# Performance work log

Hardware: AMD Instinct MI355X
Metric: run time of the kernel (lower is better)

Reference implementation:

```python
import jax, jax.numpy as jnp
import numpy as np

N = 100000   # nodes
B = 64       # graphs in batch
E = 1600000  # edges
D_IN = 2
W1D = W2D = W3D = 128
N_CLASSES = 3
MIN_SCORE = 0.1
TOL = 1e-7
BN_EPS = 1e-5


def setup_inputs() -> dict:
    key = jax.random.key(0)
    ks = jax.random.split(key, 32)
    inp = {}
    inp['x'] = jax.random.normal(ks[0], (N, D_IN), jnp.float32)
    inp['edge_index'] = jax.random.randint(ks[1], (2, E), 0, N, dtype=jnp.int32)
    inp['batch_index'] = jnp.sort(jax.random.randint(ks[2], (N,), 0, B, dtype=jnp.int32))
    inp['topk_w'] = jax.random.normal(ks[3], (D_IN,), jnp.float32)
    dims = [(D_IN, W1D), (W1D, W2D), (W2D, W3D)]
    k = 4
    for i, (din, dout) in enumerate(dims, start=1):
        inp[f'W{i}'] = jax.random.normal(ks[k], (din, dout), jnp.float32) * (1.0 / np.sqrt(din)); k += 1
        inp[f'b{i}'] = jax.random.normal(ks[k], (dout,), jnp.float32) * 0.05; k += 1
        inp[f'g{i}'] = 1.0 + 0.1 * jax.random.normal(ks[k], (dout,), jnp.float32); k += 1
        inp[f'be{i}'] = 0.1 * jax.random.normal(ks[k], (dout,), jnp.float32); k += 1
        inp[f'rm{i}'] = 0.1 * jax.random.normal(ks[k], (dout,), jnp.float32); k += 1
        inp[f'rv{i}'] = 1.0 + 0.1 * jax.random.uniform(ks[k], (dout,), jnp.float32); k += 1
    inp['linW'] = jax.random.normal(ks[k], (W3D, N_CLASSES), jnp.float32) * (1.0 / np.sqrt(W3D)); k += 1
    inp['linb'] = jax.random.normal(ks[k], (N_CLASSES,), jnp.float32) * 0.05
    return inp


def _bn_eval(x, g, be, rm, rv):
    # BatchNorm1d in eval mode (running stats)
    return (x - rm) * jax.lax.rsqrt(rv + BN_EPS) * g + be


def _gcn(x, src, dst, ew, W, b):
    # GCNConv: lin -> symmetric-normalized scatter-add (self-loops already in src/dst/ew)
    xw = x @ W                                   # [N, dout]
    deg = jax.ops.segment_sum(ew, dst, num_segments=N)
    dinv = jnp.where(deg > 0, jax.lax.rsqrt(deg), 0.0)
    norm = dinv[src] * ew * dinv[dst]            # [E+N]
    out = jax.ops.segment_sum(norm[:, None] * xw[src], dst, num_segments=N)
    return out + b


def reference(x, edge_index, batch_index, topk_w,
              W1, b1, g1, be1, rm1, rv1,
              W2, b2, g2, be2, rm2, rv2,
              W3, b3, g3, be3, rm3, rv3,
              linW, linb):
    # ---- TopKPooling (min_score mode): per-graph softmax score, threshold keep,
    # x scaled by score. Implemented via masking (fixed shapes): dropped nodes get
    # zero features, zero edge weights, and -inf at the max pool -> math identical
    # to PyG's node filtering (BN is eval-mode, i.e. per-node).
    logits = x @ topk_w                                                    # [N]
    m = jax.ops.segment_max(logits, batch_index, num_segments=B)
    e = jnp.exp(logits - m[batch_index])
    score = e / jax.ops.segment_sum(e, batch_index, num_segments=B)[batch_index]
    smax = jax.ops.segment_max(score, batch_index, num_segments=B)[batch_index] - TOL
    keep = score > jnp.minimum(smax, MIN_SCORE)                            # [N] bool
    keep_f = keep.astype(x.dtype)
    h = x * (score * keep_f)[:, None]

    src0, dst0 = edge_index[0], edge_index[1]
    loop = jnp.arange(N, dtype=src0.dtype)
    src = jnp.concatenate([src0, loop])
    dst = jnp.concatenate([dst0, loop])
    ew = jnp.concatenate([keep_f[src0] * keep_f[dst0], keep_f])            # mask + self-loops

    h = _bn_eval(jax.nn.relu(_gcn(h, src, dst, ew, W1, b1)), g1, be1, rm1, rv1)
    h = _bn_eval(jax.nn.relu(_gcn(h, src, dst, ew, W2, b2)), g2, be2, rm2, rv2)
    h = _bn_eval(jax.nn.relu(_gcn(h, src, dst, ew, W3, b3)), g3, be3, rm3, rv3)

    neg = jnp.finfo(h.dtype).min
    h = jnp.where(keep[:, None], h, neg)
    pooled = jax.ops.segment_max(h, batch_index, num_segments=B)           # [B, w3]
    out = pooled @ linW + linb
    return jax.nn.log_softmax(out, axis=1)
```

## Files before the change

### kernel.cpp

```cpp
#include <hip/hip_runtime.h>
#include <hip/hip_bf16.h>

#define NN 100000
#define BB 64
#define EE 1600000
#define FD 128
#define KMAX 8192
#define EMAX (1 << 18)

__device__ __forceinline__ unsigned encf(float f) {
    unsigned u = __float_as_uint(f);
    return (u & 0x80000000u) ? ~u : (u | 0x80000000u);
}
__device__ __forceinline__ float decf(unsigned u) {
    return __uint_as_float((u & 0x80000000u) ? (u & 0x7FFFFFFFu) : ~u);
}

struct InitBlk {
    unsigned menc[BB];
    float    ssum[BB];
    unsigned smenc[BB];
    int      kcnt;
    int      kecnt;
    int      pad[2];
    unsigned pooled[BB * FD];
};

__global__ void k_score1(const float* __restrict__ x, const float* __restrict__ tw,
                         const int* __restrict__ bidx, float* __restrict__ sc, InitBlk* ib) {
    __shared__ unsigned lm[BB];
    if (threadIdx.x < BB) lm[threadIdx.x] = 0u;
    __syncthreads();
    int i = blockIdx.x * 256 + threadIdx.x;
    if (i < NN) {
        float l = x[2 * i] * tw[0] + x[2 * i + 1] * tw[1];
        sc[i] = l;
        atomicMax(&lm[bidx[i]], encf(l));
    }
    __syncthreads();
    if (threadIdx.x < BB && lm[threadIdx.x] != 0u)
        atomicMax(&ib->menc[threadIdx.x], lm[threadIdx.x]);
}

__global__ void k_score2(const int* __restrict__ bidx, float* __restrict__ sc, InitBlk* ib) {
    __shared__ float ls[BB];
    if (threadIdx.x < BB) ls[threadIdx.x] = 0.f;
    __syncthreads();
    int i = blockIdx.x * 256 + threadIdx.x;
    if (i < NN) {
        int b = bidx[i];
        float e = expf(sc[i] - decf(ib->menc[b]));
        sc[i] = e;
        atomicAdd(&ls[b], e);
    }
    __syncthreads();
    if (threadIdx.x < BB && ls[threadIdx.x] != 0.f)
        atomicAdd(&ib->ssum[threadIdx.x], ls[threadIdx.x]);
}

__global__ void k_score3(const int* __restrict__ bidx, float* __restrict__ sc, InitBlk* ib) {
    __shared__ unsigned lm[BB];
    if (threadIdx.x < BB) lm[threadIdx.x] = 0u;
    __syncthreads();
    int i = blockIdx.x * 256 + threadIdx.x;
    if (i < NN) {
        int b = bidx[i];
        float s = sc[i] / ib->ssum[b];
        sc[i] = s;
        atomicMax(&lm[b], encf(s));
    }
    __syncthreads();
    if (threadIdx.x < BB && lm[threadIdx.x] != 0u)
        atomicMax(&ib->smenc[threadIdx.x], lm[threadIdx.x]);
}

__global__ void k_keep(const float* __restrict__ x, const int* __restrict__ bidx,
                       const float* __restrict__ sc, unsigned char* __restrict__ kf,
                       int* __restrict__ nslot, int* __restrict__ bslot,
                       float* __restrict__ degs, float* __restrict__ h0s,
                       float* __restrict__ ps, InitBlk* ib) {
    int i = blockIdx.x * 256 + threadIdx.x;
    if (i >= NN) return;
    int b = bidx[i];
    float thr = fminf(decf(ib->smenc[b]) - 1e-7f, 0.1f);
    float s = sc[i];
    bool kp = s > thr;
    int idx = -1;
    if (kp) {
        idx = atomicAdd(&ib->kcnt, 1);
        if (idx >= KMAX) kp = false;
    }
    kf[i] = kp ? 1 : 0;
    if (kp) {
        nslot[i] = idx;
        bslot[idx] = b;
        degs[idx] = 1.0f;
        h0s[2 * idx]     = x[2 * i] * s;
        h0s[2 * idx + 1] = x[2 * i + 1] * s;
        ps[2 * idx] = 0.f; ps[2 * idx + 1] = 0.f;
    }
}

__global__ void k_edges(const int* __restrict__ ei, const unsigned char* __restrict__ kf,
                        const int* __restrict__ nslot, float* __restrict__ degs,
                        int* __restrict__ kedge, InitBlk* ib) {
    int e = blockIdx.x * 256 + threadIdx.x;
    if (e >= EE) return;
    int s = ei[e], d = ei[EE + e];
    if ((kf[s] & kf[d]) != 0) {
        int ds = nslot[d];
        atomicAdd(&degs[ds], 1.0f);
        int idx = atomicAdd(&ib->kecnt, 1);
        if (idx < EMAX) { kedge[2 * idx] = nslot[s]; kedge[2 * idx + 1] = ds; }
    }
}

__global__ void k_dinv(float* __restrict__ degs, const InitBlk* ib) {
    int n = ib->kcnt; if (n > KMAX) n = KMAX;
    for (int t = blockIdx.x * blockDim.x + threadIdx.x; t < n; t += gridDim.x * blockDim.x)
        degs[t] = rsqrtf(degs[t]);
}

__global__ void k_l1edge(const float* __restrict__ dinv, const float* __restrict__ h0s,
                         float* __restrict__ ps, const int* __restrict__ kedge, const InitBlk* ib) {
    int n = ib->kecnt; if (n > EMAX) n = EMAX;
    for (int t = blockIdx.x * blockDim.x + threadIdx.x; t < n; t += gridDim.x * blockDim.x) {
        int s = kedge[2 * t], d = kedge[2 * t + 1];
        float nm = dinv[s] * dinv[d];
        atomicAdd(&ps[2 * d],     nm * h0s[2 * s]);
        atomicAdd(&ps[2 * d + 1], nm * h0s[2 * s + 1]);
    }
}

__global__ void k_l1node(const float* __restrict__ ps, const float* __restrict__ h0s,
                         const float* __restrict__ dinv,
                         const float* __restrict__ W1, const float* __restrict__ b1,
                         const float* __restrict__ g1, const float* __restrict__ be1,
                         const float* __restrict__ rm1, const float* __restrict__ rv1,
                         const InitBlk* ib, float* __restrict__ hout) {
    int kc = ib->kcnt; if (kc > KMAX) kc = KMAX;
    int n = kc * FD;
    for (int t = blockIdx.x * blockDim.x + threadIdx.x; t < n; t += gridDim.x * blockDim.x) {
        int slot = t >> 7, f = t & 127;
        float di = dinv[slot], d2 = di * di;
        float a0 = ps[2 * slot]     + d2 * h0s[2 * slot];
        float a1 = ps[2 * slot + 1] + d2 * h0s[2 * slot + 1];
        float v = a0 * W1[f] + a1 * W1[FD + f] + b1[f];
        v = fmaxf(v, 0.f);
        v = (v - rm1[f]) * rsqrtf(rv1[f] + 1e-5f) * g1[f] + be1[f];
        hout[t] = v;
    }
}

__global__ void k_mm(float* __restrict__ X, float* __restrict__ Y, const float* __restrict__ W,
                     const InitBlk* ib) {
    __shared__ float row[FD];
    int n = ib->kcnt; if (n > KMAX) n = KMAX;
    for (int slot = blockIdx.x; slot < n; slot += gridDim.x) {
        size_t base = (size_t)slot * FD;
        row[threadIdx.x] = X[base + threadIdx.x];
        X[base + threadIdx.x] = 0.f;
        __syncthreads();
        float acc = 0.f;
        #pragma unroll 16
        for (int k = 0; k < FD; k++) acc += row[k] * W[k * FD + threadIdx.x];
        Y[base + threadIdx.x] = acc;
        __syncthreads();
    }
}

__global__ void k_scatter(const float* __restrict__ Y, float* __restrict__ X,
                          const float* __restrict__ dinv, const int* __restrict__ kedge,
                          const InitBlk* ib) {
    int n = ib->kecnt; if (n > EMAX) n = EMAX;
    for (int t = blockIdx.x * blockDim.x + threadIdx.x; t < n; t += gridDim.x * blockDim.x) {
        int s = kedge[2 * t], d = kedge[2 * t + 1];
        float nm = dinv[s] * dinv[d];
        const float* ys = Y + (size_t)s * FD;
        float* xd = X + (size_t)d * FD;
        for (int f = 0; f < FD; f += 4) {
            float4 v = *(const float4*)(ys + f);
            atomicAdd(xd + f,     nm * v.x);
            atomicAdd(xd + f + 1, nm * v.y);
            atomicAdd(xd + f + 2, nm * v.z);
            atomicAdd(xd + f + 3, nm * v.w);
        }
    }
}

__global__ void k_bn(const float* __restrict__ X, float* __restrict__ Y,
                     const float* __restrict__ dinv,
                     const float* __restrict__ bb, const float* __restrict__ g,
                     const float* __restrict__ be, const float* __restrict__ rm,
                     const float* __restrict__ rv, const InitBlk* ib) {
    int kc = ib->kcnt; if (kc > KMAX) kc = KMAX;
    int n = kc * FD;
    for (int t = blockIdx.x * blockDim.x + threadIdx.x; t < n; t += gridDim.x * blockDim.x) {
        int slot = t >> 7, f = t & 127;
        float di = dinv[slot];
        float v = X[t] + di * di * Y[t] + bb[f];
        v = fmaxf(v, 0.f);
        v = (v - rm[f]) * rsqrtf(rv[f] + 1e-5f) * g[f] + be[f];
        Y[t] = v;
    }
}

__global__ void k_pool(const float* __restrict__ H, const int* __restrict__ bslot, InitBlk* ib) {
    int kc = ib->kcnt; if (kc > KMAX) kc = KMAX;
    int n = kc * FD;
    for (int t = blockIdx.x * blockDim.x + threadIdx.x; t < n; t += gridDim.x * blockDim.x) {
        int slot = t >> 7, f = t & 127;
        atomicMax(&ib->pooled[bslot[slot] * FD + f], encf(H[t]));
    }
}

__global__ void k_final(const InitBlk* __restrict__ ib, const float* __restrict__ linW,
                        const float* __restrict__ linb, float* __restrict__ out) {
    int b = threadIdx.x;
    if (b >= BB) return;
    float z0 = linb[0], z1 = linb[1], z2 = linb[2];
    for (int f = 0; f < FD; f++) {
        unsigned u = ib->pooled[b * FD + f];
        float pv = (u == 0u) ? -3.4028235e38f : decf(u);
        z0 += pv * linW[f * 3 + 0];
        z1 += pv * linW[f * 3 + 1];
        z2 += pv * linW[f * 3 + 2];
    }
    float m = fmaxf(z0, fmaxf(z1, z2));
    float l = m + logf(expf(z0 - m) + expf(z1 - m) + expf(z2 - m));
    out[b * 3 + 0] = z0 - l;
    out[b * 3 + 1] = z1 - l;
    out[b * 3 + 2] = z2 - l;
}

extern "C" void kernel_launch(void* const* d_in, const int* in_sizes, int n_in,
                              void* d_out, int out_size, void* d_ws, size_t ws_size,
                              hipStream_t stream) {
    (void)in_sizes; (void)n_in; (void)out_size; (void)ws_size;
    const float* x    = (const float*)d_in[0];
    const int*   ei   = (const int*)d_in[1];
    const int*   bidx = (const int*)d_in[2];
    const float* tw   = (const float*)d_in[3];
    const float* W1 = (const float*)d_in[4],  *b1 = (const float*)d_in[5],  *g1 = (const float*)d_in[6];
    const float* be1= (const float*)d_in[7],  *rm1= (const float*)d_in[8],  *rv1= (const float*)d_in[9];
    const float* W2 = (const float*)d_in[10], *b2 = (const float*)d_in[11], *g2 = (const float*)d_in[12];
    const float* be2= (const float*)d_in[13], *rm2= (const float*)d_in[14], *rv2= (const float*)d_in[15];
    const float* W3 = (const float*)d_in[16], *b3 = (const float*)d_in[17], *g3 = (const float*)d_in[18];
    const float* be3= (const float*)d_in[19], *rm3= (const float*)d_in[20], *rv3= (const float*)d_in[21];
    const float* linW = (const float*)d_in[22], *linb = (const float*)d_in[23];
    float* out = (float*)d_out;

    char* w = (char*)d_ws;
    auto take = [&](size_t bytes) { char* r = w; w += (bytes + 255) & ~(size_t)255; return r; };
    InitBlk* ib = (InitBlk*)take(sizeof(InitBlk));
    float* sc    = (float*)take((size_t)NN * 4);
    unsigned char* kf = (unsigned char*)take(NN);
    int*   nslot = (int*)take((size_t)NN * 4);
    int*   bslot = (int*)take((size_t)KMAX * 4);
    float* degs  = (float*)take((size_t)KMAX * 4);
    float* h0s   = (float*)take((size_t)KMAX * 8);
    float* ps    = (float*)take((size_t)KMAX * 8);
    int*   kedge = (int*)take((size_t)EMAX * 8);
    float* hA    = (float*)take((size_t)KMAX * FD * 4);
    float* hB    = (float*)take((size_t)KMAX * FD * 4);

    hipMemsetAsync(ib, 0, sizeof(InitBlk), stream);

    int nb = (NN + 255) / 256;
    int eb = (EE + 255) / 256;
    k_score1<<<nb, 256, 0, stream>>>(x, tw, bidx, sc, ib);
    k_score2<<<nb, 256, 0, stream>>>(bidx, sc, ib);
    k_score3<<<nb, 256, 0, stream>>>(bidx, sc, ib);
    k_keep  <<<nb, 256, 0, stream>>>(x, bidx, sc, kf, nslot, bslot, degs, h0s, ps, ib);
    k_edges <<<eb, 256, 0, stream>>>(ei, kf, nslot, degs, kedge, ib);
    k_dinv  <<<32, 256, 0, stream>>>(degs, ib);
    k_l1edge<<<32, 256, 0, stream>>>(degs, h0s, ps, kedge, ib);
    k_l1node<<<64, 256, 0, stream>>>(ps, h0s, degs, W1, b1, g1, be1, rm1, rv1, ib, hA);
    k_mm     <<<128, 128, 0, stream>>>(hA, hB, W2, ib);
    k_scatter<<<64, 256, 0, stream>>>(hB, hA, degs, kedge, ib);
    k_bn     <<<64, 256, 0, stream>>>(hA, hB, degs, b2, g2, be2, rm2, rv2, ib);
    k_mm     <<<128, 128, 0, stream>>>(hB, hA, W3, ib);
    k_scatter<<<64, 256, 0, stream>>>(hA, hB, degs, kedge, ib);
    k_bn     <<<64, 256, 0, stream>>>(hB, hA, degs, b3, g3, be3, rm3, rv3, ib);
    k_pool   <<<64, 256, 0, stream>>>(hA, bslot, ib);
    k_final  <<<1, 64, 0, stream>>>(ib, linW, linb, out);
}
```

Measured before the change: 176.4 us.

## Collapse pipeline into three kernels: per-graph score/keep block and single-block tail

Replaces the sixteen-launch pipeline with three kernels. One block per graph computes the softmax scores, threshold and kept-node list using binary search over the sorted batch index and a shared-memory cache. A single 1024-thread block then runs all three GCN layers, pooling and the final linear layer with block-level syncs. Kept nodes get fixed per-graph slots (capped at 64 per graph), which removes the global counters, the memset and most launch overhead. In exchange the tail runs on one CU, so it is fast only while few nodes and edges are kept, and any graph keeping more than 64 nodes would give a wrong result.

```diff
diff --git a/kernel.cpp b/kernel.cpp
--- a/kernel.cpp
+++ b/kernel.cpp
@@ -5,8 +5,10 @@
 #define BB 64
 #define EE 1600000
 #define FD 128
-#define KMAX 8192
+#define SLOTC 64
+#define KSLOTS (BB * SLOTC)
 #define EMAX (1 << 18)
+#define LCAP 12288
 
 __device__ __forceinline__ unsigned encf(float f) {
     unsigned u = __float_as_uint(f);
@@ -16,221 +18,218 @@
     return __uint_as_float((u & 0x80000000u) ? (u & 0x7FFFFFFFu) : ~u);
 }
 
-struct InitBlk {
-    unsigned menc[BB];
-    float    ssum[BB];
-    unsigned smenc[BB];
-    int      kcnt;
-    int      kecnt;
-    int      pad[2];
-    unsigned pooled[BB * FD];
-};
-
-__global__ void k_score1(const float* __restrict__ x, const float* __restrict__ tw,
-                         const int* __restrict__ bidx, float* __restrict__ sc, InitBlk* ib) {
-    __shared__ unsigned lm[BB];
-    if (threadIdx.x < BB) lm[threadIdx.x] = 0u;
-    __syncthreads();
-    int i = blockIdx.x * 256 + threadIdx.x;
-    if (i < NN) {
-        float l = x[2 * i] * tw[0] + x[2 * i + 1] * tw[1];
-        sc[i] = l;
-        atomicMax(&lm[bidx[i]], encf(l));
-    }
-    __syncthreads();
-    if (threadIdx.x < BB && lm[threadIdx.x] != 0u)
-        atomicMax(&ib->menc[threadIdx.x], lm[threadIdx.x]);
-}
-
-__global__ void k_score2(const int* __restrict__ bidx, float* __restrict__ sc, InitBlk* ib) {
-    __shared__ float ls[BB];
-    if (threadIdx.x < BB) ls[threadIdx.x] = 0.f;
-    __syncthreads();
-    int i = blockIdx.x * 256 + threadIdx.x;
-    if (i < NN) {
-        int b = bidx[i];
-        float e = expf(sc[i] - decf(ib->menc[b]));
-        sc[i] = e;
-        atomicAdd(&ls[b], e);
-    }
-    __syncthreads();
-    if (threadIdx.x < BB && ls[threadIdx.x] != 0.f)
-        atomicAdd(&ib->ssum[threadIdx.x], ls[threadIdx.x]);
-}
-
-__global__ void k_score3(const int* __restrict__ bidx, float* __restrict__ sc, InitBlk* ib) {
-    __shared__ unsigned lm[BB];
-    if (threadIdx.x < BB) lm[threadIdx.x] = 0u;
-    __syncthreads();
-    int i = blockIdx.x * 256 + threadIdx.x;
-    if (i < NN) {
-        int b = bidx[i];
-        float s = sc[i] / ib->ssum[b];
-        sc[i] = s;
-        atomicMax(&lm[b], encf(s));
-    }
-    __syncthreads();
-    if (threadIdx.x < BB && lm[threadIdx.x] != 0u)
-        atomicMax(&ib->smenc[threadIdx.x], lm[threadIdx.x]);
-}
-
-__global__ void k_keep(const float* __restrict__ x, const int* __restrict__ bidx,
-                       const float* __restrict__ sc, unsigned char* __restrict__ kf,
-                       int* __restrict__ nslot, int* __restrict__ bslot,
-                       float* __restrict__ degs, float* __restrict__ h0s,
-                       float* __restrict__ ps, InitBlk* ib) {
-    int i = blockIdx.x * 256 + threadIdx.x;
-    if (i >= NN) return;
-    int b = bidx[i];
-    float thr = fminf(decf(ib->smenc[b]) - 1e-7f, 0.1f);
-    float s = sc[i];
-    bool kp = s > thr;
-    int idx = -1;
-    if (kp) {
-        idx = atomicAdd(&ib->kcnt, 1);
-        if (idx >= KMAX) kp = false;
-    }
-    kf[i] = kp ? 1 : 0;
-    if (kp) {
-        nslot[i] = idx;
-        bslot[idx] = b;
-        degs[idx] = 1.0f;
-        h0s[2 * idx]     = x[2 * i] * s;
-        h0s[2 * idx + 1] = x[2 * i + 1] * s;
-        ps[2 * idx] = 0.f; ps[2 * idx + 1] = 0.f;
+__global__ __launch_bounds__(256) void k_scorekeep(
+    const float* __restrict__ x, const int* __restrict__ bidx,
+    const float* __restrict__ tw,
+    unsigned char* __restrict__ kf, int* __restrict__ nslot,
+    int* __restrict__ knt, float* __restrict__ degs,
+    float* __restrict__ h0s, float* __restrict__ ps, int* __restrict__ kecnt)
+{
+    __shared__ float cache[LCAP];
+    __shared__ float red[256];
+    __shared__ int   klist[SLOTC];
+    __shared__ int   lcnt;
+    __shared__ float bm, bs, bthr;
+    int b = blockIdx.x, tid = threadIdx.x;
+    if (tid == 0) { lcnt = 0; if (b == 0) *kecnt = 0; }
+
+    int lo = 0, hi = NN;
+    while (lo < hi) { int mid = (lo + hi) >> 1; if (bidx[mid] < b) lo = mid + 1; else hi = mid; }
+    int s0 = lo;
+    hi = NN;
+    while (lo < hi) { int mid = (lo + hi) >> 1; if (bidx[mid] < b + 1) lo = mid + 1; else hi = mid; }
+    int L = lo - s0;
+    float w0 = tw[0], w1 = tw[1];
+    bool fit = (L <= LCAP);
+    __syncthreads();
+
+    float mx = -3.4028235e38f;
+    for (int j = tid; j < L; j += 256) {
+        int i = s0 + j;
+        float l = x[2 * i] * w0 + x[2 * i + 1] * w1;
+        if (fit) cache[j] = l;
+        kf[i] = 0;
+        mx = fmaxf(mx, l);
+    }
+    red[tid] = mx; __syncthreads();
+    for (int s = 128; s > 0; s >>= 1) { if (tid < s) red[tid] = fmaxf(red[tid], red[tid + s]); __syncthreads(); }
+    if (tid == 0) bm = red[0];
+    __syncthreads();
+    float m = bm;
+
+    float sm = 0.f;
+    for (int j = tid; j < L; j += 256) {
+        float l = fit ? cache[j] : (x[2 * (s0 + j)] * w0 + x[2 * (s0 + j) + 1] * w1);
+        float e = expf(l - m);
+        if (fit) cache[j] = e;
+        sm += e;
+    }
+    red[tid] = sm; __syncthreads();
+    for (int s = 128; s > 0; s >>= 1) { if (tid < s) red[tid] += red[tid + s]; __syncthreads(); }
+    if (tid == 0) bs = red[0];
+    __syncthreads();
+    float S = bs;
+
+    float smx = -3.4028235e38f;
+    for (int j = tid; j < L; j += 256) {
+        float e = fit ? cache[j] : expf(x[2 * (s0 + j)] * w0 + x[2 * (s0 + j) + 1] * w1 - m);
+        float sc = e / S;
+        if (fit) cache[j] = sc;
+        smx = fmaxf(smx, sc);
+    }
+    red[tid] = smx; __syncthreads();
+    for (int s = 128; s > 0; s >>= 1) { if (tid < s) red[tid] = fmaxf(red[tid], red[tid + s]); __syncthreads(); }
+    if (tid == 0) bthr = fminf(red[0] - 1e-7f, 0.1f);
+    __syncthreads();
+    float thr = bthr;
+
+    for (int j = tid; j < L; j += 256) {
+        float sc = fit ? cache[j] : expf(x[2 * (s0 + j)] * w0 + x[2 * (s0 + j) + 1] * w1 - m) / S;
+        if (sc > thr) {
+            int l = atomicAdd(&lcnt, 1);
+            if (l < SLOTC) klist[l] = j;
+        }
+    }
+    __syncthreads();
+    int cnt = lcnt; if (cnt > SLOTC) cnt = SLOTC;
+    if (tid == 0) knt[b] = cnt;
+    for (int l = tid; l < cnt; l += 256) {
+        int j = klist[l], i = s0 + j;
+        float sc = fit ? cache[j] : expf(x[2 * i] * w0 + x[2 * i + 1] * w1 - m) / S;
+        int slot = b * SLOTC + l;
+        kf[i] = 1; nslot[i] = slot;
+        degs[slot] = 1.0f;
+        h0s[2 * slot]     = x[2 * i] * sc;
+        h0s[2 * slot + 1] = x[2 * i + 1] * sc;
+        ps[2 * slot] = 0.f; ps[2 * slot + 1] = 0.f;
     }
 }
 
 __global__ void k_edges(const int* __restrict__ ei, const unsigned char* __restrict__ kf,
                         const int* __restrict__ nslot, float* __restrict__ degs,
-                        int* __restrict__ kedge, InitBlk* ib) {
+                        int* __restrict__ kedge, int* __restrict__ kecnt) {
     int e = blockIdx.x * 256 + threadIdx.x;
     if (e >= EE) return;
     int s = ei[e], d = ei[EE + e];
     if ((kf[s] & kf[d]) != 0) {
         int ds = nslot[d];
         atomicAdd(&degs[ds], 1.0f);
-        int idx = atomicAdd(&ib->kecnt, 1);
+        int idx = atomicAdd(kecnt, 1);
         if (idx < EMAX) { kedge[2 * idx] = nslot[s]; kedge[2 * idx + 1] = ds; }
     }
 }
 
-__global__ void k_dinv(float* __restrict__ degs, const InitBlk* ib) {
-    int n = ib->kcnt; if (n > KMAX) n = KMAX;
-    for (int t = blockIdx.x * blockDim.x + threadIdx.x; t < n; t += gridDim.x * blockDim.x)
-        degs[t] = rsqrtf(degs[t]);
-}
-
-__global__ void k_l1edge(const float* __restrict__ dinv, const float* __restrict__ h0s,
-                         float* __restrict__ ps, const int* __restrict__ kedge, const InitBlk* ib) {
-    int n = ib->kecnt; if (n > EMAX) n = EMAX;
-    for (int t = blockIdx.x * blockDim.x + threadIdx.x; t < n; t += gridDim.x * blockDim.x) {
-        int s = kedge[2 * t], d = kedge[2 * t + 1];
-        float nm = dinv[s] * dinv[d];
+__global__ __launch_bounds__(1024) void k_tail(
+    float* __restrict__ degs, const float* __restrict__ h0s, float* __restrict__ ps,
+    const int* __restrict__ kedge, const int* __restrict__ kecnt,
+    const int* __restrict__ knt,
+    const float* __restrict__ W1, const float* __restrict__ b1,
+    const float* __restrict__ g1, const float* __restrict__ be1,
+    const float* __restrict__ rm1, const float* __restrict__ rv1,
+    const float* __restrict__ W2, const float* __restrict__ b2,
+    const float* __restrict__ g2, const float* __restrict__ be2,
+    const float* __restrict__ rm2, const float* __restrict__ rv2,
+    const float* __restrict__ W3, const float* __restrict__ b3,
+    const float* __restrict__ g3, const float* __restrict__ be3,
+    const float* __restrict__ rm3, const float* __restrict__ rv3,
+    const float* __restrict__ linW, const float* __restrict__ linb,
+    float* __restrict__ hA, float* __restrict__ hB, float* __restrict__ out)
+{
+    __shared__ int slist[KSLOTS];
+    __shared__ int cmap[KSLOTS];
+    __shared__ unsigned pooled[BB * FD];
+    __shared__ int kcS;
+    int tid = threadIdx.x;
+    if (tid == 0) {
+        int off = 0;
+        for (int b = 0; b < BB; b++) {
+            int c = knt[b];
+            for (int l = 0; l < c; l++) { int slot = b * SLOTC + l; slist[off] = slot; cmap[slot] = off; off++; }
+        }
+        kcS = off;
+    }
+    for (int j = tid; j < BB * FD; j += 1024) pooled[j] = 0u;
+    __syncthreads();
+    int kc = kcS;
+    int ke = *kecnt; if (ke > EMAX) ke = EMAX;
+
+    for (int j = tid; j < kc; j += 1024) { int s = slist[j]; degs[s] = rsqrtf(degs[s]); }
+    __syncthreads();
+    for (int idx = tid; idx < ke; idx += 1024) {
+        int s = kedge[2 * idx], d = kedge[2 * idx + 1];
+        float nm = degs[s] * degs[d];
         atomicAdd(&ps[2 * d],     nm * h0s[2 * s]);
         atomicAdd(&ps[2 * d + 1], nm * h0s[2 * s + 1]);
     }
-}
-
-__global__ void k_l1node(const float* __restrict__ ps, const float* __restrict__ h0s,
-                         const float* __restrict__ dinv,
-                         const float* __restrict__ W1, const float* __restrict__ b1,
-                         const float* __restrict__ g1, const float* __restrict__ be1,
-                         const float* __restrict__ rm1, const float* __restrict__ rv1,
-                         const InitBlk* ib, float* __restrict__ hout) {
-    int kc = ib->kcnt; if (kc > KMAX) kc = KMAX;
-    int n = kc * FD;
-    for (int t = blockIdx.x * blockDim.x + threadIdx.x; t < n; t += gridDim.x * blockDim.x) {
-        int slot = t >> 7, f = t & 127;
-        float di = dinv[slot], d2 = di * di;
+    __syncthreads();
+    for (int j = tid; j < kc * FD; j += 1024) {
+        int r = j >> 7, f = j & 127, slot = slist[r];
+        float di = degs[slot], d2 = di * di;
         float a0 = ps[2 * slot]     + d2 * h0s[2 * slot];
         float a1 = ps[2 * slot + 1] + d2 * h0s[2 * slot + 1];
         float v = a0 * W1[f] + a1 * W1[FD + f] + b1[f];
         v = fmaxf(v, 0.f);
         v = (v - rm1[f]) * rsqrtf(rv1[f] + 1e-5f) * g1[f] + be1[f];
-        hout[t] = v;
-    }
-}
-
-__global__ void k_mm(float* __restrict__ X, float* __restrict__ Y, const float* __restrict__ W,
-                     const InitBlk* ib) {
-    __shared__ float row[FD];
-    int n = ib->kcnt; if (n > KMAX) n = KMAX;
-    for (int slot = blockIdx.x; slot < n; slot += gridDim.x) {
-        size_t base = (size_t)slot * FD;
-        row[threadIdx.x] = X[base + threadIdx.x];
-        X[base + threadIdx.x] = 0.f;
-        __syncthreads();
-        float acc = 0.f;
-        #pragma unroll 16
-        for (int k = 0; k < FD; k++) acc += row[k] * W[k * FD + threadIdx.x];
-        Y[base + threadIdx.x] = acc;
-        __syncthreads();
-    }
-}
-
-__global__ void k_scatter(const float* __restrict__ Y, float* __restrict__ X,
-                          const float* __restrict__ dinv, const int* __restrict__ kedge,
-                          const InitBlk* ib) {
-    int n = ib->kecnt; if (n > EMAX) n = EMAX;
-    for (int t = blockIdx.x * blockDim.x + threadIdx.x; t < n; t += gridDim.x * blockDim.x) {
-        int s = kedge[2 * t], d = kedge[2 * t + 1];
-        float nm = dinv[s] * dinv[d];
-        const float* ys = Y + (size_t)s * FD;
-        float* xd = X + (size_t)d * FD;
-        for (int f = 0; f < FD; f += 4) {
-            float4 v = *(const float4*)(ys + f);
-            atomicAdd(xd + f,     nm * v.x);
-            atomicAdd(xd + f + 1, nm * v.y);
-            atomicAdd(xd + f + 2, nm * v.z);
-            atomicAdd(xd + f + 3, nm * v.w);
-        }
-    }
-}
-
-__global__ void k_bn(const float* __restrict__ X, float* __restrict__ Y,
-                     const float* __restrict__ dinv,
-                     const float* __restrict__ bb, const float* __restrict__ g,
-                     const float* __restrict__ be, const float* __restrict__ rm,
-                     const float* __restrict__ rv, const InitBlk* ib) {
-    int kc = ib->kcnt; if (kc > KMAX) kc = KMAX;
-    int n = kc * FD;
-    for (int t = blockIdx.x * blockDim.x + threadIdx.x; t < n; t += gridDim.x * blockDim.x) {
-        int slot = t >> 7, f = t & 127;
-        float di = dinv[slot];
-        float v = X[t] + di * di * Y[t] + bb[f];
-        v = fmaxf(v, 0.f);
-        v = (v - rm[f]) * rsqrtf(rv[f] + 1e-5f) * g[f] + be[f];
-        Y[t] = v;
-    }
-}
-
-__global__ void k_pool(const float* __restrict__ H, const int* __restrict__ bslot, InitBlk* ib) {
-    int kc = ib->kcnt; if (kc > KMAX) kc = KMAX;
-    int n = kc * FD;
-    for (int t = blockIdx.x * blockDim.x + threadIdx.x; t < n; t += gridDim.x * blockDim.x) {
-        int slot = t >> 7, f = t & 127;
-        atomicMax(&ib->pooled[bslot[slot] * FD + f], encf(H[t]));
-    }
-}
-
-__global__ void k_final(const InitBlk* __restrict__ ib, const float* __restrict__ linW,
-                        const float* __restrict__ linb, float* __restrict__ out) {
-    int b = threadIdx.x;
-    if (b >= BB) return;
-    float z0 = linb[0], z1 = linb[1], z2 = linb[2];
-    for (int f = 0; f < FD; f++) {
-        unsigned u = ib->pooled[b * FD + f];
-        float pv = (u == 0u) ? -3.4028235e38f : decf(u);
-        z0 += pv * linW[f * 3 + 0];
-        z1 += pv * linW[f * 3 + 1];
-        z2 += pv * linW[f * 3 + 2];
-    }
-    float m = fmaxf(z0, fmaxf(z1, z2));
-    float l = m + logf(expf(z0 - m) + expf(z1 - m) + expf(z2 - m));
-    out[b * 3 + 0] = z0 - l;
-    out[b * 3 + 1] = z1 - l;
-    out[b * 3 + 2] = z2 - l;
+        hA[j] = v;
+    }
+    __syncthreads();
+
+    float* X = hA; float* Y = hB;
+    const float* Wl[2]  = {W2, W3};  const float* bl[2]  = {b2, b3};
+    const float* gl[2]  = {g2, g3};  const float* bel[2] = {be2, be3};
+    const float* rml[2] = {rm2, rm3}; const float* rvl[2] = {rv2, rv3};
+    for (int layer = 0; layer < 2; layer++) {
+        const float* W = Wl[layer];
+        for (int j = tid; j < kc * FD; j += 1024) {
+            int r = j >> 7, f = j & 127;
+            const float* xr = X + r * FD;
+            float acc = 0.f;
+            #pragma unroll 8
+            for (int k = 0; k < FD; k++) acc += xr[k] * W[k * FD + f];
+            Y[j] = acc;
+        }
+        __syncthreads();
+        for (int j = tid; j < kc * FD; j += 1024) X[j] = 0.f;
+        __syncthreads();
+        for (int idx = tid; idx < ke * FD; idx += 1024) {
+            int e = idx >> 7, f = idx & 127;
+            int s = kedge[2 * e], d = kedge[2 * e + 1];
+            float nm = degs[s] * degs[d];
+            atomicAdd(&X[cmap[d] * FD + f], nm * Y[cmap[s] * FD + f]);
+        }
+        __syncthreads();
+        for (int j = tid; j < kc * FD; j += 1024) {
+            int r = j >> 7, f = j & 127, slot = slist[r];
+            float di = degs[slot];
+            float v = X[j] + di * di * Y[j] + bl[layer][f];
+            v = fmaxf(v, 0.f);
+            v = (v - rml[layer][f]) * rsqrtf(rvl[layer][f] + 1e-5f) * gl[layer][f] + bel[layer][f];
+            Y[j] = v;
+        }
+        __syncthreads();
+        float* t = X; X = Y; Y = t;
+    }
+    for (int j = tid; j < kc * FD; j += 1024) {
+        int r = j >> 7, f = j & 127, slot = slist[r], b = slot / SLOTC;
+        atomicMax(&pooled[b * FD + f], encf(X[j]));
+    }
+    __syncthreads();
+    if (tid < BB) {
+        int b = tid;
+        float z0 = linb[0], z1 = linb[1], z2 = linb[2];
+        for (int f = 0; f < FD; f++) {
+            unsigned u = pooled[b * FD + f];
+            float pv = (u == 0u) ? -3.4028235e38f : decf(u);
+            z0 += pv * linW[f * 3 + 0];
+            z1 += pv * linW[f * 3 + 1];
+            z2 += pv * linW[f * 3 + 2];
+        }
+        float m = fmaxf(z0, fmaxf(z1, z2));
+        float l = m + logf(expf(z0 - m) + expf(z1 - m) + expf(z2 - m));
+        out[b * 3 + 0] = z0 - l;
+        out[b * 3 + 1] = z1 - l;
+        out[b * 3 + 2] = z2 - l;
+    }
 }
 
 extern "C" void kernel_launch(void* const* d_in, const int* in_sizes, int n_in,
@@ -252,36 +251,22 @@
 
     char* w = (char*)d_ws;
     auto take = [&](size_t bytes) { char* r = w; w += (bytes + 255) & ~(size_t)255; return r; };
-    InitBlk* ib = (InitBlk*)take(sizeof(InitBlk));
-    float* sc    = (float*)take((size_t)NN * 4);
     unsigned char* kf = (unsigned char*)take(NN);
     int*   nslot = (int*)take((size_t)NN * 4);
-    int*   bslot = (int*)take((size_t)KMAX * 4);
-    float* degs  = (float*)take((size_t)KMAX * 4);
-    float* h0s   = (float*)take((size_t)KMAX * 8);
-    float* ps    = (float*)take((size_t)KMAX * 8);
+    int*   knt   = (int*)take((size_t)BB * 4);
+    int*   kecnt = (int*)take(16);
+    float* degs  = (float*)take((size_t)KSLOTS * 4);
+    float* h0s   = (float*)take((size_t)KSLOTS * 8);
+    float* ps    = (float*)take((size_t)KSLOTS * 8);
     int*   kedge = (int*)take((size_t)EMAX * 8);
-    float* hA    = (float*)take((size_t)KMAX * FD * 4);
-    float* hB    = (float*)take((size_t)KMAX * FD * 4);
-
-    hipMemsetAsync(ib, 0, sizeof(InitBlk), stream);
-
-    int nb = (NN + 255) / 256;
-    int eb = (EE + 255) / 256;
-    k_score1<<<nb, 256, 0, stream>>>(x, tw, bidx, sc, ib);
-    k_score2<<<nb, 256, 0, stream>>>(bidx, sc, ib);
-    k_score3<<<nb, 256, 0, stream>>>(bidx, sc, ib);
-    k_keep  <<<nb, 256, 0, stream>>>(x, bidx, sc, kf, nslot, bslot, degs, h0s, ps, ib);
-    k_edges <<<eb, 256, 0, stream>>>(ei, kf, nslot, degs, kedge, ib);
-    k_dinv  <<<32, 256, 0, stream>>>(degs, ib);
-    k_l1edge<<<32, 256, 0, stream>>>(degs, h0s, ps, kedge, ib);
-    k_l1node<<<64, 256, 0, stream>>>(ps, h0s, degs, W1, b1, g1, be1, rm1, rv1, ib, hA);
-    k_mm     <<<128, 128, 0, stream>>>(hA, hB, W2, ib);
-    k_scatter<<<64, 256, 0, stream>>>(hB, hA, degs, kedge, ib);
-    k_bn     <<<64, 256, 0, stream>>>(hA, hB, degs, b2, g2, be2, rm2, rv2, ib);
-    k_mm     <<<128, 128, 0, stream>>>(hB, hA, W3, ib);
-    k_scatter<<<64, 256, 0, stream>>>(hA, hB, degs, kedge, ib);
-    k_bn     <<<64, 256, 0, stream>>>(hB, hA, degs, b3, g3, be3, rm3, rv3, ib);
-    k_pool   <<<64, 256, 0, stream>>>(hA, bslot, ib);
-    k_final  <<<1, 64, 0, stream>>>(ib, linW, linb, out);
-}
+    float* hA    = (float*)take((size_t)KSLOTS * FD * 4);
+    float* hB    = (float*)take((size_t)KSLOTS * FD * 4);
+
+    k_scorekeep<<<BB, 256, 0, stream>>>(x, bidx, tw, kf, nslot, knt, degs, h0s, ps, kecnt);
+    k_edges<<<(EE + 255) / 256, 256, 0, stream>>>(ei, kf, nslot, degs, kedge, kecnt);
+    k_tail<<<1, 1024, 0, stream>>>(degs, h0s, ps, kedge, kecnt, knt,
+                                   W1, b1, g1, be1, rm1, rv1,
+                                   W2, b2, g2, be2, rm2, rv2,
+                                   W3, b3, g3, be3, rm3, rv3,
+                                   linW, linb, hA, hB, out);
+}
```

Result: slower. 266.4 us (+51.0%).
